# Performance work log

Measured on AMD Instinct MI355X. Metric: run time of the kernel, lower is better.

Reference implementation:

```python
import jax, jax.numpy as jnp
import numpy as np

N_TYPES = 4  # global / and / or / leaf node types (indep_weights)


def gcn_layer(x, W_stack, b, edge_src, edge_dst, edge_w, labels, num_nodes):
    # Per-node-type dense projection: compute all 4 projections, then select by label.
    # all4: [4, N, out]
    all4 = jnp.einsum('nd,kdo->kno', x, W_stack)
    support = jnp.take_along_axis(all4, labels[None, :, None].astype(jnp.int32), axis=0)[0]  # [N, out]
    # Sparse adjacency propagation: out[dst] += w * support[src]  (torch.spmm equivalent)
    msgs = support[edge_src] * edge_w[:, None]  # [E, out]
    agg = jax.ops.segment_sum(msgs, edge_dst, num_segments=num_nodes)
    return agg + b


def setup_inputs() -> dict:
    key = jax.random.key(0)
    ks = jax.random.split(key, 12)
    N, E = 50000, 1600000
    nfeat, nhid, nclass = 256, 256, 64
    x = jax.random.normal(ks[0], (N, nfeat), dtype=jnp.float32)
    edge_src = jax.random.randint(ks[1], (E,), 0, N, dtype=jnp.int32)
    edge_dst = jax.random.randint(ks[2], (E,), 0, N, dtype=jnp.int32)
    edge_w = jax.random.uniform(ks[3], (E,), dtype=jnp.float32)
    labels = jax.random.randint(ks[4], (N,), 0, N_TYPES, dtype=jnp.int32)
    def winit(k, fi, fo):
        s = 1.0 / np.sqrt(fo)
        return jax.random.uniform(k, (N_TYPES, fi, fo), minval=-s, maxval=s, dtype=jnp.float32)
    def binit(k, fo):
        s = 1.0 / np.sqrt(fo)
        return jax.random.uniform(k, (fo,), minval=-s, maxval=s, dtype=jnp.float32)
    return {
        'x': x, 'edge_src': edge_src, 'edge_dst': edge_dst, 'edge_w': edge_w, 'labels': labels,
        'W1': winit(ks[5], nfeat, nhid), 'b1': binit(ks[6], nhid),
        'W2': winit(ks[7], nhid, nhid), 'b2': binit(ks[8], nhid),
        'W3': winit(ks[9], nhid, nclass), 'b3': binit(ks[10], nclass),
    }


def reference(x, edge_src, edge_dst, edge_w, labels, W1, b1, W2, b2, W3, b3):
    N = x.shape[0]
    h = jax.nn.relu(gcn_layer(x, W1, b1, edge_src, edge_dst, edge_w, labels, N))
    # F.dropout with p=0 (module default) is identity
    h = jax.nn.relu(gcn_layer(h, W2, b2, edge_src, edge_dst, edge_w, labels, N))
    out = gcn_layer(h, W3, b3, edge_src, edge_dst, edge_w, labels, N)
    return out
```

## Files before the change

### kernel.cpp

```cpp
#include <hip/hip_runtime.h>
#include <hip/hip_bf16.h>

#define NT 4
#define FEAT 256
#define OUT3 64

typedef __bf16 bf16x8 __attribute__((ext_vector_type(8)));
typedef float  f32x4  __attribute__((ext_vector_type(4)));
typedef unsigned int u32x2 __attribute__((ext_vector_type(2)));

__device__ inline unsigned int f2bf_bits(float f) {
    __hip_bfloat16 h = __float2bfloat16(f);
    unsigned short u;
    __builtin_memcpy(&u, &h, 2);
    return (unsigned int)u;
}
__device__ inline float bfl(unsigned int u) { return __uint_as_float(u << 16); }
__device__ inline float bfh(unsigned int u) { return __uint_as_float(u & 0xffff0000u); }
__device__ __host__ inline int nat_of(int p) {
    int lo = p & 63;
    return (p & ~63) | (((lo & 3) << 4) | (lo >> 2));
}

__global__ __launch_bounds__(512) void pass_a(const int* __restrict__ dst,
                                              const int* __restrict__ labels,
                                              int* __restrict__ bcnt, int* __restrict__ lc,
                                              int E, int N) {
    __shared__ int h[256];
    __shared__ int lh[NT];
    int tid = threadIdx.x;
    if (tid < 256) h[tid] = 0;
    if (tid < NT) lh[tid] = 0;
    __syncthreads();
    int base = blockIdx.x * 4096;
#pragma unroll
    for (int k = 0; k < 8; ++k) {
        int e = base + k * 512 + tid;
        if (e < E) atomicAdd(&h[((unsigned)dst[e]) >> 8], 1);
    }
#pragma unroll
    for (int k = 0; k < 8; ++k) {
        int i = base + k * 512 + tid;
        if (i < N) atomicAdd(&lh[labels[i]], 1);
    }
    __syncthreads();
    if (tid < 256) { int v = h[tid]; if (v) atomicAdd(&bcnt[tid], v); }
    if (tid < NT) { int v = lh[tid]; if (v) atomicAdd(&lc[tid], v); }
}

__global__ __launch_bounds__(256) void scan_master(
    const int* __restrict__ bcnt, const int* __restrict__ lc,
    int* __restrict__ boff, int* __restrict__ gcur, int* __restrict__ rowoff,
    int* __restrict__ lstart, int NB, int N, int E) {
    __shared__ int s[256];
    int tid = threadIdx.x;
    int own = (tid < NB) ? bcnt[tid] : 0;
    s[tid] = own;
    __syncthreads();
    for (int d = 1; d < 256; d <<= 1) {
        int v = (tid >= d) ? s[tid - d] : 0;
        __syncthreads();
        s[tid] += v;
        __syncthreads();
    }
    int excl = s[tid] - own;
    if (tid < NB) { boff[tid] = excl; gcur[tid] = excl; }
    if (tid == 0) {
        boff[NB] = E; rowoff[N] = E;
        int run = 0;
        for (int l = 0; l < NT; ++l) {
            lstart[l] = run;
            run += (lc[l] + 63) & ~63;
        }
    }
}

__global__ void scatter_nodes(const int* __restrict__ labels, const int* __restrict__ lstart,
                              int* __restrict__ lcur, int* __restrict__ iperm, int N) {
    int n = blockIdx.x * 256 + threadIdx.x;
    int lab = (n < N) ? labels[n] : -1;
    int lane = threadIdx.x & 63;
    for (int l = 0; l < NT; ++l) {
        unsigned long long m = __ballot(lab == l);
        if (m == 0ull) continue;
        int leader = __builtin_ctzll(m);
        int base = 0;
        if (lane == leader) base = atomicAdd(&lcur[l], (int)__popcll(m));
        base = __shfl(base, leader, 64);
        if (lab == l) {
            int prefix = (int)__popcll(m & ((1ull << lane) - 1ull));
            iperm[n] = lstart[l] + base + prefix;
        }
    }
}

__global__ __launch_bounds__(512) void fuse_a(
    const int* __restrict__ src, const int* __restrict__ dst, const float* __restrict__ w,
    const int* __restrict__ iperm, int* __restrict__ gcur, uint2* __restrict__ earr, int E,
    const float* __restrict__ x, unsigned short* __restrict__ act, int total4,
    const float* __restrict__ W1, const float* __restrict__ W2, const float* __restrict__ W3,
    const float* __restrict__ b1, const float* __restrict__ b2,
    unsigned short* __restrict__ W1b, unsigned short* __restrict__ W2b,
    unsigned short* __restrict__ W3b, float* __restrict__ biasPerm,
    int nbEB, int nbX) {
    int tid = threadIdx.x;
    int blk = (int)blockIdx.x;
    if (blk < nbEB) {
        __shared__ int h[256];
        __shared__ int basearr[256];
        if (tid < 256) h[tid] = 0;
        __syncthreads();
        int base = blk * 4096;
        int b[8], rank[8], px[8]; float wv[8];
#pragma unroll
        for (int k = 0; k < 8; ++k) {
            int e = base + k * 512 + tid;
            if (e < E) {
                int d = dst[e];
                b[k] = ((unsigned)d) >> 8;
                px[k] = iperm[src[e]] | ((d & 255) << 16);
                wv[k] = w[e];
                rank[k] = atomicAdd(&h[b[k]], 1);
            } else b[k] = -1;
        }
        __syncthreads();
        if (tid < 256) { int c = h[tid]; basearr[tid] = c ? atomicAdd(&gcur[tid], c) : 0; }
        __syncthreads();
#pragma unroll
        for (int k = 0; k < 8; ++k) {
            if (b[k] >= 0) {
                int pos = basearr[b[k]] + rank[k];
                earr[pos] = make_uint2((unsigned)px[k], __float_as_uint(wv[k]));
            }
        }
    } else if (blk < nbEB + nbX) {
        int i = (blk - nbEB) * 512 + tid;
        if (i < total4) {
            float4 v = ((const float4*)x)[i];
            unsigned int lo = f2bf_bits(v.x) | (f2bf_bits(v.y) << 16);
            unsigned int hi = f2bf_bits(v.z) | (f2bf_bits(v.w) << 16);
            int slot = iperm[i >> 6];
            ((uint2*)act)[(size_t)slot * 64 + (i & 63)] = make_uint2(lo, hi);
        }
    } else {
        const int S = NT * FEAT * FEAT;
        const int S3 = NT * FEAT * OUT3;
        int idx = (blk - nbEB - nbX) * 512 + tid;
        if (idx < 2 * S + S3) {
            const float* W; unsigned short* D; int OUTF; int t; bool remap;
            if (idx < S)          { W = W1; D = W1b; OUTF = FEAT; t = idx;         remap = false; }
            else if (idx < 2 * S) { W = W2; D = W2b; OUTF = FEAT; t = idx - S;     remap = true; }
            else                  { W = W3; D = W3b; OUTF = OUT3; t = idx - 2 * S; remap = true; }
            int n = t % OUTF;
            int r = t / OUTF;
            int j = r & 7, q = (r >> 3) & 3, k0 = (r >> 5) & 7, lab = r >> 8;
            int k_slot = k0 * 32 + q * 8 + j;
            int k_src = remap ? nat_of(k_slot) : k_slot;
            float f = W[((size_t)(lab * FEAT + k_src)) * OUTF + n];
            D[(((size_t)lab * 8 + k0) * OUTF + n) * 32 + q * 8 + j] = (unsigned short)f2bf_bits(f);
        } else {
            int p2 = idx - (2 * S + S3);
            if (p2 < 256) biasPerm[p2] = b1[nat_of(p2)];
            else if (p2 < 512) biasPerm[p2] = b2[nat_of(p2 - 256)];
        }
    }
}

__device__ void bucket_sort_body(int b, const uint2* __restrict__ earr,
                                 const int* __restrict__ boff, int* __restrict__ rowoff,
                                 unsigned int* __restrict__ edata, int N) {
    int s = boff[b], e = boff[b + 1];
    __shared__ int cnt[256], off[256];
    int tid = threadIdx.x;
    cnt[tid] = 0;
    __syncthreads();
    for (int i = s + tid; i < e; i += 256) atomicAdd(&cnt[(earr[i].x >> 16) & 255], 1);
    __syncthreads();
    off[tid] = cnt[tid];
    __syncthreads();
    for (int d = 1; d < 256; d <<= 1) {
        int v = (tid >= d) ? off[tid - d] : 0;
        __syncthreads();
        off[tid] += v;
        __syncthreads();
    }
    int excl = off[tid] - cnt[tid];
    int node = b * 256 + tid;
    if (node < N) rowoff[node] = s + excl;
    off[tid] = excl;
    __syncthreads();
    for (int i = s + tid; i < e; i += 256) {
        uint2 r = earr[i];
        int d = (r.x >> 16) & 255;
        int k = atomicAdd(&off[d], 1);
        edata[s + k] = (f2bf_bits(__uint_as_float(r.y)) << 16) | (r.x & 0xffff);
    }
}

__device__ void proj256_body(int gb,
                             const unsigned short* __restrict__ act,
                             const unsigned short* __restrict__ Wswz,
                             const int* __restrict__ lstart,
                             unsigned short* __restrict__ sup) {
    int warp = threadIdx.x >> 6;
    int lane = threadIdx.x & 63;
    int m0 = gb * 64;
    int lab = (m0 >= lstart[1]) + (m0 >= lstart[2]) + (m0 >= lstart[3]);
    int q = lane >> 4, c = lane & 15;
    int n0 = warp * 64;

    const unsigned short* arow = act + (size_t)(m0 + c) * 256 + q * 8;
    const unsigned short* bb = Wswz + (size_t)lab * FEAT * 256 + (size_t)(n0 + c) * 32 + q * 8;

    f32x4 acc[4][4] = {};
#pragma unroll
    for (int k0 = 0; k0 < 8; ++k0) {
        const unsigned short* abase = arow + ((k0 & 3) * 32) + ((k0 < 4) ? 0 : 128);
        bf16x8 a[4];
#pragma unroll
        for (int t = 0; t < 4; ++t) a[t] = *(const bf16x8*)(abase + (size_t)t * 4096);
        const unsigned short* bk = bb + (size_t)k0 * 32 * 256;
#pragma unroll
        for (int u = 0; u < 4; ++u) {
            bf16x8 bfrag = *(const bf16x8*)(bk + u * 512);
#pragma unroll
            for (int t = 0; t < 4; ++t)
                acc[t][u] = __builtin_amdgcn_mfma_f32_16x16x32_bf16(a[t], bfrag, acc[t][u], 0, 0, 0);
        }
    }
    uint2* ov = (uint2*)sup;
    int cix = (n0 >> 2) + c;
#pragma unroll
    for (int t = 0; t < 4; ++t) {
#pragma unroll
        for (int r = 0; r < 4; ++r) {
            int row = m0 + t * 16 + q * 4 + r;
            unsigned int lo = f2bf_bits(acc[t][0][r]) | (f2bf_bits(acc[t][1][r]) << 16);
            unsigned int hi = f2bf_bits(acc[t][2][r]) | (f2bf_bits(acc[t][3][r]) << 16);
            ov[(size_t)row * 64 + cix] = make_uint2(lo, hi);
        }
    }
}

__global__ __launch_bounds__(256) void fuse_b(
    const uint2* __restrict__ earr, const int* __restrict__ boff,
    int* __restrict__ rowoff, unsigned int* __restrict__ edata, int N, int NB,
    const unsigned short* __restrict__ act,
    const unsigned short* __restrict__ Wswz, const int* __restrict__ lstart,
    unsigned short* __restrict__ sup) {
    int blk = (int)blockIdx.x;
    if (blk < NB) bucket_sort_body(blk, earr, boff, rowoff, edata, N);
    else proj256_body(blk - NB, act, Wswz, lstart, sup);
}

__global__ __launch_bounds__(256) void proj256_kernel(
    const unsigned short* __restrict__ act,
    const unsigned short* __restrict__ Wswz, const int* __restrict__ lstart,
    unsigned short* __restrict__ sup) {
    proj256_body((int)blockIdx.x, act, Wswz, lstart, sup);
}

__global__ __launch_bounds__(256) void proj64_kernel(
    const unsigned short* __restrict__ act,
    const unsigned short* __restrict__ Wswz, const int* __restrict__ lstart,
    unsigned short* __restrict__ outp) {
    int warp = threadIdx.x >> 6;
    int lane = threadIdx.x & 63;
    int m0 = blockIdx.x * 64;
    int lab = (m0 >= lstart[1]) + (m0 >= lstart[2]) + (m0 >= lstart[3]);
    int q = lane >> 4, c = lane & 15;
    int mb = m0 + warp * 16;

    const unsigned short* arow = act + (size_t)(mb + c) * 256 + q * 8;
    const unsigned short* bb = Wswz + (size_t)lab * FEAT * OUT3 + (size_t)c * 32 + q * 8;

    f32x4 acc[4] = {};
#pragma unroll
    for (int k0 = 0; k0 < 8; ++k0) {
        bf16x8 a = *(const bf16x8*)(arow + ((k0 & 3) * 32) + ((k0 < 4) ? 0 : 128));
        const unsigned short* bk = bb + (size_t)k0 * 32 * OUT3;
#pragma unroll
        for (int u = 0; u < 4; ++u) {
            bf16x8 bfrag = *(const bf16x8*)(bk + u * 512);
            acc[u] = __builtin_amdgcn_mfma_f32_16x16x32_bf16(a, bfrag, acc[u], 0, 0, 0);
        }
    }
    uint2* ov = (uint2*)outp;
#pragma unroll
    for (int r = 0; r < 4; ++r) {
        int row = mb + q * 4 + r;
        unsigned int lo = f2bf_bits(acc[0][r]) | (f2bf_bits(acc[1][r]) << 16);
        unsigned int hi = f2bf_bits(acc[2][r]) | (f2bf_bits(acc[3][r]) << 16);
        ov[(size_t)row * 16 + c] = make_uint2(lo, hi);
    }
}

__global__ __launch_bounds__(256) void agg256_kernel(
    const uint2* __restrict__ sup, const int* __restrict__ rowoff,
    const unsigned int* __restrict__ edata, const int* __restrict__ iperm,
    const float* __restrict__ bias, u32x2* __restrict__ outp, int N) {
    int warp = __builtin_amdgcn_readfirstlane((int)(threadIdx.x >> 6));
    int node = (int)blockIdx.x * 4 + warp;
    if (node >= N) return;
    int lane = threadIdx.x & 63;
    int s = __builtin_amdgcn_readfirstlane(rowoff[node]);
    int e = __builtin_amdgcn_readfirstlane(rowoff[node + 1]);
    int slot = __builtin_amdgcn_readfirstlane(iperm[node]);
    float a0 = 0.f, a1 = 0.f, a2 = 0.f, a3 = 0.f;
    int j = s;
    for (; j + 8 <= e; j += 8) {
        unsigned int ed[8]; uint2 v[8];
#pragma unroll
        for (int u = 0; u < 8; ++u) ed[u] = edata[j + u];
#pragma unroll
        for (int u = 0; u < 8; ++u) v[u] = sup[(size_t)(ed[u] & 0xffff) * 64 + lane];
#pragma unroll
        for (int u = 0; u < 8; ++u) {
            float w = __uint_as_float(ed[u] & 0xffff0000u);
            a0 += w * bfl(v[u].x); a1 += w * bfh(v[u].x);
            a2 += w * bfl(v[u].y); a3 += w * bfh(v[u].y);
        }
    }
    if (j < e) {
        unsigned int ed[8]; uint2 v[8]; float wm[8];
#pragma unroll
        for (int u = 0; u < 8; ++u) {
            int jj = j + u;
            int jc = (jj < e) ? jj : e - 1;
            ed[u] = edata[jc];
            wm[u] = (jj < e) ? __uint_as_float(ed[u] & 0xffff0000u) : 0.f;
        }
#pragma unroll
        for (int u = 0; u < 8; ++u) v[u] = sup[(size_t)(ed[u] & 0xffff) * 64 + lane];
#pragma unroll
        for (int u = 0; u < 8; ++u) {
            a0 += wm[u] * bfl(v[u].x); a1 += wm[u] * bfh(v[u].x);
            a2 += wm[u] * bfl(v[u].y); a3 += wm[u] * bfh(v[u].y);
        }
    }
    float4 b = ((const float4*)bias)[lane];
    a0 = fmaxf(a0 + b.x, 0.f);
    a1 = fmaxf(a1 + b.y, 0.f);
    a2 = fmaxf(a2 + b.z, 0.f);
    a3 = fmaxf(a3 + b.w, 0.f);
    u32x2 o;
    o[0] = f2bf_bits(a0) | (f2bf_bits(a1) << 16);
    o[1] = f2bf_bits(a2) | (f2bf_bits(a3) << 16);
    __builtin_nontemporal_store(o, &outp[(size_t)slot * 64 + lane]);
}

__global__ __launch_bounds__(256) void agg64_kernel(
    const unsigned short* __restrict__ sup, const int* __restrict__ rowoff,
    const unsigned int* __restrict__ edata, const float* __restrict__ b3,
    float* __restrict__ outp, int N) {
    int warp = __builtin_amdgcn_readfirstlane((int)(threadIdx.x >> 6));
    int node = (int)blockIdx.x * 4 + warp;
    if (node >= N) return;
    int lane = threadIdx.x & 63;
    int s = __builtin_amdgcn_readfirstlane(rowoff[node]);
    int e = __builtin_amdgcn_readfirstlane(rowoff[node + 1]);
    float a = 0.f;
    int j = s;
    for (; j + 8 <= e; j += 8) {
        unsigned int ed[8]; unsigned short v[8];
#pragma unroll
        for (int u = 0; u < 8; ++u) ed[u] = edata[j + u];
#pragma unroll
        for (int u = 0; u < 8; ++u) v[u] = sup[(size_t)(ed[u] & 0xffff) * 64 + lane];
#pragma unroll
        for (int u = 0; u < 8; ++u)
            a += __uint_as_float(ed[u] & 0xffff0000u) * __uint_as_float((unsigned int)v[u] << 16);
    }
    if (j < e) {
        unsigned int ed[8]; float wm[8]; unsigned short v[8];
#pragma unroll
        for (int u = 0; u < 8; ++u) {
            int jj = j + u;
            int jc = (jj < e) ? jj : e - 1;
            ed[u] = edata[jc];
            wm[u] = (jj < e) ? __uint_as_float(ed[u] & 0xffff0000u) : 0.f;
        }
#pragma unroll
        for (int u = 0; u < 8; ++u) v[u] = sup[(size_t)(ed[u] & 0xffff) * 64 + lane];
#pragma unroll
        for (int u = 0; u < 8; ++u)
            a += wm[u] * __uint_as_float((unsigned int)v[u] << 16);
    }
    int natp = (((lane & 3) << 4) | (lane >> 2));
    outp[(size_t)node * 64 + natp] = a + b3[natp];
}

extern "C" void kernel_launch(void* const* d_in, const int* in_sizes, int n_in,
                              void* d_out, int out_size, void* d_ws, size_t ws_size,
                              hipStream_t stream) {
    const float* x        = (const float*)d_in[0];
    const int*   edge_src = (const int*)d_in[1];
    const int*   edge_dst = (const int*)d_in[2];
    const float* edge_w   = (const float*)d_in[3];
    const int*   labels   = (const int*)d_in[4];
    const float* W1 = (const float*)d_in[5];
    const float* b1 = (const float*)d_in[6];
    const float* W2 = (const float*)d_in[7];
    const float* b2 = (const float*)d_in[8];
    const float* W3 = (const float*)d_in[9];
    const float* b3 = (const float*)d_in[10];

    const int N = in_sizes[0] / FEAT;
    const int E = in_sizes[1];
    const int NB = (N + 255) >> 8;
    const int G64 = (N + NT * 64 + 63) / 64;
    const int slotCap = G64 * 64;

    char* p = (char*)d_ws;
    auto alloc = [&](size_t bytes) -> char* {
        char* r = p;
        p += (bytes + 255) & ~(size_t)255;
        return r;
    };
    unsigned short* bufA = (unsigned short*)alloc((size_t)slotCap * FEAT * 2);
    unsigned short* bufB = (unsigned short*)alloc((size_t)slotCap * FEAT * 2);
    unsigned short* W1b  = (unsigned short*)alloc((size_t)NT * FEAT * FEAT * 2);
    unsigned short* W2b  = (unsigned short*)alloc((size_t)NT * FEAT * FEAT * 2);
    unsigned short* W3b  = (unsigned short*)alloc((size_t)NT * FEAT * OUT3 * 2);
    float*        biasPerm = (float*)alloc(512 * 4);
    int*          rowoff = (int*)alloc((size_t)(N + 1) * 4);
    unsigned int* edata  = (unsigned int*)alloc((size_t)E * 4);
    int*          iperm  = (int*)alloc((size_t)N * 4);
    int*          counters = (int*)alloc(264 * 4);
    int*          boff   = (int*)alloc(257 * 4);
    int*          gcur   = (int*)alloc(256 * 4);
    int*          lstart = (int*)alloc(64);
    int* bcnt = counters;
    int* lc   = counters + 256;
    int* lcur = counters + 260;

    unsigned short* act = bufA;
    unsigned short* sup = bufB;
    uint2* earr = (uint2*)d_out;

    const int nbEB = (E + 4095) / 4096;
    const int total4 = N * 64;
    const int nbX = (total4 + 511) / 512;
    const int totW = 2 * NT * FEAT * FEAT + NT * FEAT * OUT3 + 512;
    const int nbW = (totW + 511) / 512;

    hipMemsetAsync(counters, 0, 264 * 4, stream);
    pass_a<<<nbEB, 512, 0, stream>>>(edge_dst, labels, bcnt, lc, E, N);
    scan_master<<<1, 256, 0, stream>>>(bcnt, lc, boff, gcur, rowoff, lstart, NB, N, E);
    scatter_nodes<<<(N + 255) / 256, 256, 0, stream>>>(labels, lstart, lcur, iperm, N);
    fuse_a<<<nbEB + nbX + nbW, 512, 0, stream>>>(
        edge_src, edge_dst, edge_w, iperm, gcur, earr, E,
        x, act, total4,
        W1, W2, W3, b1, b2, W1b, W2b, W3b, biasPerm, nbEB, nbX);

    const int aggGrid = (N + 3) / 4;
    fuse_b<<<NB + G64, 256, 0, stream>>>(earr, boff, rowoff, edata, N, NB,
                                         act, W1b, lstart, sup);
    agg256_kernel<<<aggGrid, 256, 0, stream>>>((const uint2*)sup, rowoff, edata, iperm,
                                               biasPerm + 0, (u32x2*)act, N);
    proj256_kernel<<<G64, 256, 0, stream>>>(act, W2b, lstart, sup);
    agg256_kernel<<<aggGrid, 256, 0, stream>>>((const uint2*)sup, rowoff, edata, iperm,
                                               biasPerm + 256, (u32x2*)act, N);
    proj64_kernel<<<G64, 256, 0, stream>>>(act, W3b, lstart, bufB);
    agg64_kernel<<<aggGrid, 256, 0, stream>>>(bufB, rowoff, edata, b3, (float*)d_out, N);
}
```

Baseline: 492.1 us.

## Sort CSR rows by source and sweep source slices across nodes per wave

Each CSR row's edges are now sorted by source slot with an insertion sort during CSR construction. The 256-wide aggregation kernel gives each wave 13 destination nodes and walks them in 16 source-index slices, so gathers at any moment hit a narrow band of the support matrix and reuse L2. The 64-wide aggregation unroll goes from 8 to 16. The cost is a serial per-thread insertion sort, one-edge-at-a-time gathers with less memory-level parallelism, and extra register pressure from 13 accumulator sets.

```diff
diff --git a/kernel.cpp b/kernel.cpp
--- a/kernel.cpp
+++ b/kernel.cpp
@@ -4,6 +4,8 @@
 #define NT 4
 #define FEAT 256
 #define OUT3 64
+#define NPW 13
+#define NSLICE 16
 
 typedef __bf16 bf16x8 __attribute__((ext_vector_type(8)));
 typedef float  f32x4  __attribute__((ext_vector_type(4)));
@@ -187,6 +189,7 @@
     int excl = off[tid] - cnt[tid];
     int node = b * 256 + tid;
     if (node < N) rowoff[node] = s + excl;
+    int rs = s + excl;
     off[tid] = excl;
     __syncthreads();
     for (int i = s + tid; i < e; i += 256) {
@@ -194,6 +197,15 @@
         int d = (r.x >> 16) & 255;
         int k = atomicAdd(&off[d], 1);
         edata[s + k] = (f2bf_bits(__uint_as_float(r.y)) << 16) | (r.x & 0xffff);
+    }
+    __syncthreads();
+    int re = s + off[tid];
+    for (int i = rs + 1; i < re; ++i) {
+        unsigned int key = edata[i];
+        unsigned int ks = key & 0xffffu;
+        int k = i - 1;
+        while (k >= rs && (edata[k] & 0xffffu) > ks) { edata[k + 1] = edata[k]; --k; }
+        edata[k + 1] = key;
     }
 }
 
@@ -295,58 +307,60 @@
     }
 }
 
-__global__ __launch_bounds__(256) void agg256_kernel(
+__global__ __launch_bounds__(256, 4) void agg256p_kernel(
     const uint2* __restrict__ sup, const int* __restrict__ rowoff,
     const unsigned int* __restrict__ edata, const int* __restrict__ iperm,
-    const float* __restrict__ bias, u32x2* __restrict__ outp, int N) {
-    int warp = __builtin_amdgcn_readfirstlane((int)(threadIdx.x >> 6));
-    int node = (int)blockIdx.x * 4 + warp;
-    if (node >= N) return;
+    const float* __restrict__ bias, u32x2* __restrict__ outp, int N, int slotCap) {
+    int wid = (int)blockIdx.x * 4 + (int)(threadIdx.x >> 6);
     int lane = threadIdx.x & 63;
-    int s = __builtin_amdgcn_readfirstlane(rowoff[node]);
-    int e = __builtin_amdgcn_readfirstlane(rowoff[node + 1]);
-    int slot = __builtin_amdgcn_readfirstlane(iperm[node]);
-    float a0 = 0.f, a1 = 0.f, a2 = 0.f, a3 = 0.f;
-    int j = s;
-    for (; j + 8 <= e; j += 8) {
-        unsigned int ed[8]; uint2 v[8];
-#pragma unroll
-        for (int u = 0; u < 8; ++u) ed[u] = edata[j + u];
-#pragma unroll
-        for (int u = 0; u < 8; ++u) v[u] = sup[(size_t)(ed[u] & 0xffff) * 64 + lane];
-#pragma unroll
-        for (int u = 0; u < 8; ++u) {
-            float w = __uint_as_float(ed[u] & 0xffff0000u);
-            a0 += w * bfl(v[u].x); a1 += w * bfh(v[u].x);
-            a2 += w * bfl(v[u].y); a3 += w * bfh(v[u].y);
-        }
-    }
-    if (j < e) {
-        unsigned int ed[8]; uint2 v[8]; float wm[8];
-#pragma unroll
-        for (int u = 0; u < 8; ++u) {
-            int jj = j + u;
-            int jc = (jj < e) ? jj : e - 1;
-            ed[u] = edata[jc];
-            wm[u] = (jj < e) ? __uint_as_float(ed[u] & 0xffff0000u) : 0.f;
-        }
-#pragma unroll
-        for (int u = 0; u < 8; ++u) v[u] = sup[(size_t)(ed[u] & 0xffff) * 64 + lane];
-#pragma unroll
-        for (int u = 0; u < 8; ++u) {
-            a0 += wm[u] * bfl(v[u].x); a1 += wm[u] * bfh(v[u].x);
-            a2 += wm[u] * bfl(v[u].y); a3 += wm[u] * bfh(v[u].y);
+    int n0 = wid * NPW;
+    if (n0 >= N) return;
+    int jj[NPW], en[NPW];
+    float a[NPW][4];
+#pragma unroll
+    for (int t = 0; t < NPW; ++t) {
+        int n = n0 + t;
+        bool ok = n < N;
+        jj[t] = ok ? __builtin_amdgcn_readfirstlane(rowoff[n]) : 0;
+        en[t] = ok ? __builtin_amdgcn_readfirstlane(rowoff[n + 1]) : 0;
+        a[t][0] = 0.f; a[t][1] = 0.f; a[t][2] = 0.f; a[t][3] = 0.f;
+    }
+    const int step = (slotCap + NSLICE - 1) / NSLICE;
+    int send = step;
+    for (int s = 0; s < NSLICE; ++s, send += step) {
+        int bound = (s == NSLICE - 1) ? 0x7fffffff : send;
+#pragma unroll
+        for (int t = 0; t < NPW; ++t) {
+            int j = jj[t], e = en[t];
+            while (j < e) {
+                unsigned int ed = edata[j];
+                int sv = __builtin_amdgcn_readfirstlane((int)(ed & 0xffffu));
+                if (sv >= bound) break;
+                uint2 v = sup[(size_t)(ed & 0xffffu) * 64 + lane];
+                float w = __uint_as_float(ed & 0xffff0000u);
+                a[t][0] += w * bfl(v.x); a[t][1] += w * bfh(v.x);
+                a[t][2] += w * bfl(v.y); a[t][3] += w * bfh(v.y);
+                ++j;
+            }
+            jj[t] = j;
         }
     }
     float4 b = ((const float4*)bias)[lane];
-    a0 = fmaxf(a0 + b.x, 0.f);
-    a1 = fmaxf(a1 + b.y, 0.f);
-    a2 = fmaxf(a2 + b.z, 0.f);
-    a3 = fmaxf(a3 + b.w, 0.f);
-    u32x2 o;
-    o[0] = f2bf_bits(a0) | (f2bf_bits(a1) << 16);
-    o[1] = f2bf_bits(a2) | (f2bf_bits(a3) << 16);
-    __builtin_nontemporal_store(o, &outp[(size_t)slot * 64 + lane]);
+#pragma unroll
+    for (int t = 0; t < NPW; ++t) {
+        int n = n0 + t;
+        if (n < N) {
+            int slot = __builtin_amdgcn_readfirstlane(iperm[n]);
+            float r0 = fmaxf(a[t][0] + b.x, 0.f);
+            float r1 = fmaxf(a[t][1] + b.y, 0.f);
+            float r2 = fmaxf(a[t][2] + b.z, 0.f);
+            float r3 = fmaxf(a[t][3] + b.w, 0.f);
+            u32x2 o;
+            o[0] = f2bf_bits(r0) | (f2bf_bits(r1) << 16);
+            o[1] = f2bf_bits(r2) | (f2bf_bits(r3) << 16);
+            __builtin_nontemporal_store(o, &outp[(size_t)slot * 64 + lane]);
+        }
+    }
 }
 
 __global__ __launch_bounds__(256) void agg64_kernel(
@@ -361,29 +375,29 @@
     int e = __builtin_amdgcn_readfirstlane(rowoff[node + 1]);
     float a = 0.f;
     int j = s;
-    for (; j + 8 <= e; j += 8) {
-        unsigned int ed[8]; unsigned short v[8];
-#pragma unroll
-        for (int u = 0; u < 8; ++u) ed[u] = edata[j + u];
-#pragma unroll
-        for (int u = 0; u < 8; ++u) v[u] = sup[(size_t)(ed[u] & 0xffff) * 64 + lane];
-#pragma unroll
-        for (int u = 0; u < 8; ++u)
+    for (; j + 16 <= e; j += 16) {
+        unsigned int ed[16]; unsigned short v[16];
+#pragma unroll
+        for (int u = 0; u < 16; ++u) ed[u] = edata[j + u];
+#pragma unroll
+        for (int u = 0; u < 16; ++u) v[u] = sup[(size_t)(ed[u] & 0xffff) * 64 + lane];
+#pragma unroll
+        for (int u = 0; u < 16; ++u)
             a += __uint_as_float(ed[u] & 0xffff0000u) * __uint_as_float((unsigned int)v[u] << 16);
     }
     if (j < e) {
-        unsigned int ed[8]; float wm[8]; unsigned short v[8];
-#pragma unroll
-        for (int u = 0; u < 8; ++u) {
-            int jj = j + u;
-            int jc = (jj < e) ? jj : e - 1;
+        unsigned int ed[16]; float wm[16]; unsigned short v[16];
+#pragma unroll
+        for (int u = 0; u < 16; ++u) {
+            int jjj = j + u;
+            int jc = (jjj < e) ? jjj : e - 1;
             ed[u] = edata[jc];
-            wm[u] = (jj < e) ? __uint_as_float(ed[u] & 0xffff0000u) : 0.f;
-        }
-#pragma unroll
-        for (int u = 0; u < 8; ++u) v[u] = sup[(size_t)(ed[u] & 0xffff) * 64 + lane];
-#pragma unroll
-        for (int u = 0; u < 8; ++u)
+            wm[u] = (jjj < e) ? __uint_as_float(ed[u] & 0xffff0000u) : 0.f;
+        }
+#pragma unroll
+        for (int u = 0; u < 16; ++u) v[u] = sup[(size_t)(ed[u] & 0xffff) * 64 + lane];
+#pragma unroll
+        for (int u = 0; u < 16; ++u)
             a += wm[u] * __uint_as_float((unsigned int)v[u] << 16);
     }
     int natp = (((lane & 3) << 4) | (lane >> 2));
@@ -453,14 +467,15 @@
         x, act, total4,
         W1, W2, W3, b1, b2, W1b, W2b, W3b, biasPerm, nbEB, nbX);
 
+    const int gridP = (N + 4 * NPW - 1) / (4 * NPW);
     const int aggGrid = (N + 3) / 4;
     fuse_b<<<NB + G64, 256, 0, stream>>>(earr, boff, rowoff, edata, N, NB,
                                          act, W1b, lstart, sup);
-    agg256_kernel<<<aggGrid, 256, 0, stream>>>((const uint2*)sup, rowoff, edata, iperm,
-                                               biasPerm + 0, (u32x2*)act, N);
+    agg256p_kernel<<<gridP, 256, 0, stream>>>((const uint2*)sup, rowoff, edata, iperm,
+                                              biasPerm + 0, (u32x2*)act, N, slotCap);
     proj256_kernel<<<G64, 256, 0, stream>>>(act, W2b, lstart, sup);
-    agg256_kernel<<<aggGrid, 256, 0, stream>>>((const uint2*)sup, rowoff, edata, iperm,
-                                               biasPerm + 256, (u32x2*)act, N);
+    agg256p_kernel<<<gridP, 256, 0, stream>>>((const uint2*)sup, rowoff, edata, iperm,
+                                              biasPerm + 256, (u32x2*)act, N, slotCap);
     proj64_kernel<<<G64, 256, 0, stream>>>(act, W3b, lstart, bufB);
     agg64_kernel<<<aggGrid, 256, 0, stream>>>(bufB, rowoff, edata, b3, (float*)d_out, N);
 }
```

Measured after the change: 1.140 ms. 2.32x slower.
